# Kernel optimization log

Hardware: AMD Instinct MI355X
Metric: run time of the kernel (lower is better)

Reference implementation:

```python
import jax, jax.numpy as jnp
import numpy as np

B, T, D = 2, 1024, 1024
NUM_HEADS_ARG = 16
HS = D // NUM_HEADS_ARG          # 64 (per-head size)
H = HS                           # bug in source: num_heads passed = head_size -> 64 heads
FF = 4 * D
EPS = 1e-5


def _layernorm(x, gamma, beta):
    mu = jnp.mean(x, axis=-1, keepdims=True)
    var = jnp.mean(jnp.square(x - mu), axis=-1, keepdims=True)
    return (x - mu) * jax.lax.rsqrt(var + EPS) * gamma + beta


def setup_inputs() -> dict:
    key = jax.random.key(0)
    ks = jax.random.split(key, 12)
    s_d = 1.0 / np.sqrt(D)
    s_cat = 1.0 / np.sqrt(H * HS)
    s_ff = 1.0 / np.sqrt(FF)
    return {
        "x": jax.random.normal(ks[0], (B, T, D), jnp.float32),
        "Wq": jax.random.uniform(ks[1], (H, D, HS), jnp.float32, -s_d, s_d),
        "Wk": jax.random.uniform(ks[2], (H, D, HS), jnp.float32, -s_d, s_d),
        "Wv": jax.random.uniform(ks[3], (H, D, HS), jnp.float32, -s_d, s_d),
        "Wo": jax.random.uniform(ks[4], (H * HS, D), jnp.float32, -s_cat, s_cat),
        "bo": jax.random.uniform(ks[5], (D,), jnp.float32, -s_cat, s_cat),
        "W1": jax.random.uniform(ks[6], (D, FF), jnp.float32, -s_d, s_d),
        "b1": jax.random.uniform(ks[7], (FF,), jnp.float32, -s_d, s_d),
        "W2": jax.random.uniform(ks[8], (FF, D), jnp.float32, -s_ff, s_ff),
        "b2": jax.random.uniform(ks[9], (D,), jnp.float32, -s_ff, s_ff),
        "g1": jnp.ones((D,), jnp.float32),
        "be1": jnp.zeros((D,), jnp.float32),
        "g2": jnp.ones((D,), jnp.float32),
        "be2": jnp.zeros((D,), jnp.float32),
    }


def reference(x, Wq, Wk, Wv, Wo, bo, W1, b1, W2, b2, g1, be1, g2, be2):
    # per-head projections (no bias): [B,H,T,hs]
    q = jnp.einsum('btd,hde->bhte', x, Wq)
    k = jnp.einsum('btd,hde->bhte', x, Wk)
    v = jnp.einsum('btd,hde->bhte', x, Wv)
    scores = jnp.einsum('bhte,bhse->bhts', q, k) / np.sqrt(HS)  # [B,H,T,T]
    causal = jnp.tril(jnp.ones((T, T), bool))
    scores = jnp.where(causal, scores, -jnp.inf)
    probs = jax.nn.softmax(scores, axis=-1)
    att = jnp.einsum('bhts,bhse->bhte', probs, v)               # [B,H,T,hs]
    # torch stack(dim=3) -> [B,T,hs,H] then flatten: index = d*H + h
    cat = jnp.transpose(att, (0, 2, 3, 1)).reshape(B, T, HS * H)
    mha = cat @ Wo + bo
    x1 = _layernorm(x + mha, g1, be1)
    ff = jax.nn.relu(x1 @ W1 + b1) @ W2 + b2
    return _layernorm(x1 + ff, g2, be2)
```

## Files before the change

kernel.cpp:

```cpp
#include <hip/hip_runtime.h>

typedef unsigned short u16;
typedef __bf16 bf16x8 __attribute__((ext_vector_type(8)));
typedef float f32x4 __attribute__((ext_vector_type(4)));

#define B_ 2
#define T_ 1024
#define D_ 1024
#define H_ 64
#define HS_ 64
#define FF_ 4096
#define SZ_QKV 8388608L
#define S_SCALE 0.1803368801111f

__device__ __forceinline__ float bf2f(u16 u) {
  union { unsigned int v; float f; } x; x.v = ((unsigned int)u) << 16; return x.f;
}
__device__ __forceinline__ u16 f2bf(float f) {
  union { float f; unsigned int v; } x; x.f = f;
  unsigned int r = x.v + 0x7fffu + ((x.v >> 16) & 1u);
  return (u16)(r >> 16);
}
__device__ __forceinline__ u16 f2bf_rtz(float f) {
  union { float f; unsigned int v; } x; x.f = f;
  return (u16)(x.v >> 16);
}

typedef __attribute__((address_space(3))) unsigned int lds_u32;
typedef __attribute__((address_space(1))) const unsigned int glb_u32;
__device__ __forceinline__ void gload_lds16(const void* g, void* l) {
  __builtin_amdgcn_global_load_lds((glb_u32*)g, (lds_u32*)l, 16, 0, 0);
}

__global__ __launch_bounds__(256) void prep(
    const float* __restrict__ x, const float* __restrict__ Wq,
    const float* __restrict__ Wk, const float* __restrict__ Wv,
    const float* __restrict__ Wo, const float* __restrict__ W1,
    const float* __restrict__ W2,
    u16* __restrict__ xb, u16* __restrict__ Wqkvt, u16* __restrict__ Wot,
    u16* __restrict__ W1t, u16* __restrict__ W2t)
{
  __shared__ float tile[64][65];
  int id = blockIdx.x;
  if (id < 1024) {
    const long i = ((long)id * 256 + threadIdx.x) * 8;
    float4 a = *(const float4*)(x + i);
    float4 b = *(const float4*)(x + i + 4);
    union { uint4 v; u16 u[8]; } o;
    o.u[0]=f2bf(a.x); o.u[1]=f2bf(a.y); o.u[2]=f2bf(a.z); o.u[3]=f2bf(a.w);
    o.u[4]=f2bf(b.x); o.u[5]=f2bf(b.y); o.u[6]=f2bf(b.z); o.u[7]=f2bf(b.w);
    *(uint4*)(xb + i) = o.v;
    return;
  }
  id -= 1024;
  const float* in; u16* out; long ibase, obase; int in_rs, out_rs, r0, c0;
  if (id < 3072) {
    const int w = id >> 10, rem = id & 1023;
    const int z = rem >> 4, rt = rem & 15;
    in = (w == 0) ? Wq : (w == 1) ? Wk : Wv;
    ibase = (long)z * 65536; in_rs = 64; r0 = rt * 64; c0 = 0;
    out = Wqkvt + (long)w * 4194304;
    obase = (long)z * 65536; out_rs = 1024;
  } else if (id < 4096) {
    const int rem = id - 3072;
    const int z = rem >> 4, ct = rem & 15;
    in = Wo; ibase = (long)z * 1024; in_rs = 65536; r0 = 0; c0 = ct * 64;
    out = Wot; obase = (long)z * 64; out_rs = 4096;
  } else if (id < 5120) {
    const int rem = id - 4096;
    const int rt = rem >> 6, ct = rem & 63;
    in = W1; ibase = 0; in_rs = 4096; r0 = rt * 64; c0 = ct * 64;
    out = W1t; obase = 0; out_rs = 1024;
  } else {
    const int rem = id - 5120;
    const int rt = rem >> 4, ct = rem & 15;
    in = W2; ibase = 0; in_rs = 1024; r0 = rt * 64; c0 = ct * 64;
    out = W2t; obase = 0; out_rs = 4096;
  }
  const int t = threadIdx.x, lr = t >> 4, lc4 = (t & 15) * 4;
  #pragma unroll
  for (int j = 0; j < 4; ++j) {
    float4 f = *(const float4*)(in + ibase + (long)(r0 + lr + j * 16) * in_rs + c0 + lc4);
    tile[lr + j * 16][lc4]     = f.x;
    tile[lr + j * 16][lc4 + 1] = f.y;
    tile[lr + j * 16][lc4 + 2] = f.z;
    tile[lr + j * 16][lc4 + 3] = f.w;
  }
  __syncthreads();
  const int cr = t >> 3, ch = t & 7;
  #pragma unroll
  for (int j2 = 0; j2 < 2; ++j2) {
    const int crr = cr + j2 * 32;
    union { uint4 v; u16 u[8]; } o;
    #pragma unroll
    for (int i = 0; i < 8; ++i) o.u[i] = f2bf(tile[ch * 8 + i][crr]);
    *(uint4*)(out + obase + (long)(c0 + crr) * out_rs + r0 + ch * 8) = o.v;
  }
}

template<int TM, int EPI>
__global__ __launch_bounds__(256) void gemm_k(
    const u16* __restrict__ A, const u16* __restrict__ Bt, u16* __restrict__ C,
    const float* __restrict__ bias, int K, int lda, int ldb, int koff, int ldc)
{
  constexpr int NR = (TM == 128) ? 4 : 2;
  constexpr int AIT = TM / 64;
  __shared__ __attribute__((aligned(16))) u16 As[TM * 32];
  __shared__ __attribute__((aligned(16))) u16 Bs[128 * 32];
  const int bm = blockIdx.x, bn = blockIdx.y, bz = blockIdx.z;
  const long ko = (long)bz * koff;
  const int tid = threadIdx.x, wave = tid >> 6, lane = tid & 63;
  const int quad = lane >> 4, l16 = lane & 15;
  const int wm = (TM == 128) ? (wave & 1) * 64 : 0;
  const int wn = (TM == 128) ? (wave >> 1) * 64 : wave * 32;

  f32x4 acc[4][NR];
  #pragma unroll
  for (int i = 0; i < 4; ++i)
    #pragma unroll
    for (int j = 0; j < NR; ++j) acc[i][j] = (f32x4){0, 0, 0, 0};

  const int nK = K >> 5;
  for (int kc = 0; kc < nK; ++kc) {
    const int k0 = kc << 5;
    #pragma unroll
    for (int jA = 0; jA < AIT; ++jA) {
      const int i = jA * 4 + wave;
      const int chunk = i * 64 + lane;
      gload_lds16(A + (long)(bm * TM + (chunk >> 2)) * lda + ko + k0 + (chunk & 3) * 8,
                  (u16*)As + i * 512);
    }
    #pragma unroll
    for (int jB = 0; jB < 2; ++jB) {
      const int i = jB * 4 + wave;
      const int chunk = i * 64 + lane;
      gload_lds16(Bt + (long)(bn * 128 + (chunk >> 2)) * ldb + ko + k0 + (chunk & 3) * 8,
                  (u16*)Bs + i * 512);
    }
    __syncthreads();
    bf16x8 a[4], b[NR];
    #pragma unroll
    for (int i = 0; i < 4; ++i)
      a[i] = *(const bf16x8*)&As[(wm + i * 16 + l16) * 32 + quad * 8];
    #pragma unroll
    for (int j = 0; j < NR; ++j)
      b[j] = *(const bf16x8*)&Bs[(wn + j * 16 + l16) * 32 + quad * 8];
    #pragma unroll
    for (int i = 0; i < 4; ++i)
      #pragma unroll
      for (int j = 0; j < NR; ++j)
        acc[i][j] = __builtin_amdgcn_mfma_f32_16x16x32_bf16(a[i], b[j], acc[i][j], 0, 0, 0);
    __syncthreads();
  }

  #pragma unroll
  for (int j = 0; j < NR; ++j) {
    const int col = bn * 128 + wn + j * 16 + l16;
    const float bval = (EPI == 0 || EPI == 1) ? bias[col] : 0.f;
    #pragma unroll
    for (int i = 0; i < 4; ++i) {
      #pragma unroll
      for (int r = 0; r < 4; ++r) {
        const int row = bm * TM + wm + i * 16 + quad * 4 + r;
        float vv = acc[i][j][r] + bval;
        if (EPI == 1) vv = fmaxf(vv, 0.f);
        if (EPI == 2) {
          const int which = col >> 12, rem = col & 4095;
          const int h = rem >> 6, e = rem & 63;
          const int bb = row >> 10, t = row & 1023;
          C[(long)which * SZ_QKV + ((long)((bb << 6) + h)) * 65536L + t * 64 + e] = f2bf(vv);
        } else if (EPI == 3) {
          ((float*)C)[(long)bz * 2097152 + (long)row * ldc + col] = vv;
        } else {
          C[(long)row * ldc + col] = f2bf(vv);
        }
      }
    }
  }
}

__global__ __launch_bounds__(256) void attn_flash(
    const u16* __restrict__ Q, const u16* __restrict__ Kg,
    const u16* __restrict__ V, u16* __restrict__ Om)
{
  __shared__ __attribute__((aligned(16))) u16 Ks[2][64][72];
  __shared__ __attribute__((aligned(16))) u16 Vs[2][64][72];
  __shared__ __attribute__((aligned(16))) u16 QP[4][16][72];
  const int bh = blockIdx.x;
  const int qt = gridDim.y - 1 - blockIdx.y;
  const int b = bh >> 6, h = bh & 63;
  const long base = (long)bh * (T_ * HS_);
  const int tid = threadIdx.x;
  const int wave = tid >> 6, lane = tid & 63, quad = lane >> 4, l16 = lane & 15;
  const int sm = tid >> 2, sc = (tid & 3) * 16;
  const int vswz = (sc >> 4) << 3;

  {
    const int qr = lane >> 3, qe = (lane & 7) * 8;
    #pragma unroll
    for (int j = 0; j < 2; ++j) {
      union { uint4 v; u16 u[8]; } a, o;
      a.v = *(const uint4*)(Q + base + (long)(qt * 64 + wave * 16 + qr + j * 8) * HS_ + qe);
      #pragma unroll
      for (int i = 0; i < 8; ++i) o.u[i] = f2bf(bf2f(a.u[i]) * S_SCALE);
      *(uint4*)&QP[wave][qr + j * 8][qe] = o.v;
    }
  }
  bf16x8 aq0 = *(const bf16x8*)&QP[wave][l16][quad * 8];
  bf16x8 aq1 = *(const bf16x8*)&QP[wave][l16][32 + quad * 8];

  float psum[4] = { 0.f, 0.f, 0.f, 0.f };
  f32x4 oacc[4] = { {0,0,0,0}, {0,0,0,0}, {0,0,0,0}, {0,0,0,0} };

  uint4 kA, kB, vA, vB;
  kA = *(const uint4*)(Kg + base + (long)sm * HS_ + sc);
  kB = *(const uint4*)(Kg + base + (long)sm * HS_ + sc + 8);
  vA = *(const uint4*)(V  + base + (long)sm * HS_ + sc);
  vB = *(const uint4*)(V  + base + (long)sm * HS_ + sc + 8);
  {
    *(uint4*)&Ks[0][sm][sc] = kA; *(uint4*)&Ks[0][sm][sc + 8] = kB;
    union { uint4 v; u16 u[8]; } t0, t1; t0.v = vA; t1.v = vB;
    #pragma unroll
    for (int i = 0; i < 8; ++i) Vs[0][sc + i][sm ^ vswz] = t0.u[i];
    #pragma unroll
    for (int i = 0; i < 8; ++i) Vs[0][sc + 8 + i][sm ^ vswz] = t1.u[i];
  }
  __syncthreads();

  for (int kt = 0; kt <= qt; ++kt) {
    const int cur = kt & 1;
    const bool pf = (kt < qt);
    if (pf) {
      const long nb = base + (long)((kt + 1) * 64 + sm) * HS_ + sc;
      kA = *(const uint4*)(Kg + nb); kB = *(const uint4*)(Kg + nb + 8);
      vA = *(const uint4*)(V  + nb); vB = *(const uint4*)(V  + nb + 8);
    }

    f32x4 sacc[4] = { {0,0,0,0}, {0,0,0,0}, {0,0,0,0}, {0,0,0,0} };
    #pragma unroll
    for (int nt = 0; nt < 4; ++nt) {
      bf16x8 b0 = *(const bf16x8*)&Ks[cur][nt * 16 + l16][quad * 8];
      bf16x8 b1 = *(const bf16x8*)&Ks[cur][nt * 16 + l16][32 + quad * 8];
      sacc[nt] = __builtin_amdgcn_mfma_f32_16x16x32_bf16(aq0, b0, sacc[nt], 0, 0, 0);
      sacc[nt] = __builtin_amdgcn_mfma_f32_16x16x32_bf16(aq1, b1, sacc[nt], 0, 0, 0);
    }

    if (kt == qt) {
      #pragma unroll
      for (int nt = 0; nt < 4; ++nt) {
        const int col = nt * 16 + l16;
        #pragma unroll
        for (int r = 0; r < 4; ++r) {
          const int row = wave * 16 + quad * 4 + r;
          float p = exp2f(sacc[nt][r]);
          p = (col <= row) ? p : 0.f;
          sacc[nt][r] = p; psum[r] += p;
        }
      }
    } else {
      #pragma unroll
      for (int nt = 0; nt < 4; ++nt)
        #pragma unroll
        for (int r = 0; r < 4; ++r) {
          const float p = exp2f(sacc[nt][r]);
          sacc[nt][r] = p; psum[r] += p;
        }
    }

    #pragma unroll
    for (int nt = 0; nt < 4; ++nt)
      #pragma unroll
      for (int r = 0; r < 4; ++r)
        QP[wave][quad * 4 + r][nt * 16 + l16] = f2bf_rtz(sacc[nt][r]);
    bf16x8 p0 = *(const bf16x8*)&QP[wave][l16][quad * 8];
    bf16x8 p1 = *(const bf16x8*)&QP[wave][l16][32 + quad * 8];

    #pragma unroll
    for (int et = 0; et < 4; ++et) {
      const int c0 = ((quad ^ et) * 8);
      bf16x8 b0 = *(const bf16x8*)&Vs[cur][et * 16 + l16][c0];
      bf16x8 b1 = *(const bf16x8*)&Vs[cur][et * 16 + l16][32 + c0];
      oacc[et] = __builtin_amdgcn_mfma_f32_16x16x32_bf16(p0, b0, oacc[et], 0, 0, 0);
      oacc[et] = __builtin_amdgcn_mfma_f32_16x16x32_bf16(p1, b1, oacc[et], 0, 0, 0);
    }

    if (pf) {
      const int nxt = 1 - cur;
      *(uint4*)&Ks[nxt][sm][sc] = kA; *(uint4*)&Ks[nxt][sm][sc + 8] = kB;
      union { uint4 v; u16 u[8]; } t0, t1; t0.v = vA; t1.v = vB;
      #pragma unroll
      for (int i = 0; i < 8; ++i) Vs[nxt][sc + i][sm ^ vswz] = t0.u[i];
      #pragma unroll
      for (int i = 0; i < 8; ++i) Vs[nxt][sc + 8 + i][sm ^ vswz] = t1.u[i];
    }
    __syncthreads();
  }

  #pragma unroll
  for (int off = 1; off < 16; off <<= 1)
    #pragma unroll
    for (int r = 0; r < 4; ++r)
      psum[r] += __shfl_xor(psum[r], off, 64);
  u16 (*Os)[72] = Ks[0];
  #pragma unroll
  for (int r = 0; r < 4; ++r) {
    const float rinv = 1.f / fmaxf(psum[r], 1e-20f);
    const int row = wave * 16 + quad * 4 + r;
    #pragma unroll
    for (int et = 0; et < 4; ++et)
      Os[row][et * 16 + l16] = f2bf(oacc[et][r] * rinv);
  }
  const int orow = wave * 16 + (lane >> 3), oe = (lane & 7) * 8;
  #pragma unroll
  for (int it = 0; it < 2; ++it) {
    const int rr = orow + it * 8;
    uint4 o = *(const uint4*)&Os[rr][oe];
    *(uint4*)(Om + ((long)(b * T_ + qt * 64 + rr)) * 4096 + h * 64 + oe) = o;
  }
}

template<int XBF, int OBF>
__global__ __launch_bounds__(256) void ln_sum4(
    const float* __restrict__ P4, const float* __restrict__ bias,
    const void* __restrict__ Xv, const float* __restrict__ g,
    const float* __restrict__ be, void* __restrict__ outv)
{
  __shared__ float red[8];
  const int row = blockIdx.x, tid = threadIdx.x;
  const long base = (long)row * D_;
  float v4[4]; float s = 0.f;
  #pragma unroll
  for (int j = 0; j < 4; ++j) {
    const int i = tid + j * 256;
    float acc = bias[i];
    #pragma unroll
    for (int p = 0; p < 4; ++p) acc += P4[(long)p * 2097152 + base + i];
    const float xval = XBF ? bf2f(((const u16*)Xv)[base + i]) : ((const float*)Xv)[base + i];
    v4[j] = xval + acc;
    s += v4[j];
  }
  #pragma unroll
  for (int off = 32; off > 0; off >>= 1) s += __shfl_down(s, off, 64);
  if ((tid & 63) == 0) red[tid >> 6] = s;
  __syncthreads();
  const float mu = (red[0] + red[1] + red[2] + red[3]) * (1.f / D_);
  float vs = 0.f;
  #pragma unroll
  for (int j = 0; j < 4; ++j) { const float d = v4[j] - mu; vs += d * d; }
  #pragma unroll
  for (int off = 32; off > 0; off >>= 1) vs += __shfl_down(vs, off, 64);
  __syncthreads();
  if ((tid & 63) == 0) red[tid >> 6] = vs;
  __syncthreads();
  const float rs = rsqrtf((red[0] + red[1] + red[2] + red[3]) * (1.f / D_) + 1e-5f);
  #pragma unroll
  for (int j = 0; j < 4; ++j) {
    const int i = tid + j * 256;
    const float o = (v4[j] - mu) * rs * g[i] + be[i];
    if (OBF) ((u16*)outv)[base + i] = f2bf(o);
    else     ((float*)outv)[base + i] = o;
  }
}

extern "C" void kernel_launch(void* const* d_in, const int* in_sizes, int n_in,
                              void* d_out, int out_size, void* d_ws, size_t ws_size,
                              hipStream_t stream) {
  const float* x   = (const float*)d_in[0];
  const float* Wq  = (const float*)d_in[1];
  const float* Wk  = (const float*)d_in[2];
  const float* Wv  = (const float*)d_in[3];
  const float* Wo  = (const float*)d_in[4];
  const float* bo  = (const float*)d_in[5];
  const float* W1  = (const float*)d_in[6];
  const float* b1  = (const float*)d_in[7];
  const float* W2  = (const float*)d_in[8];
  const float* b2  = (const float*)d_in[9];
  const float* g1  = (const float*)d_in[10];
  const float* be1 = (const float*)d_in[11];
  const float* g2  = (const float*)d_in[12];
  const float* be2 = (const float*)d_in[13];
  float* out = (float*)d_out;

  u16* ws = (u16*)d_ws;
  u16* xb    = ws;
  u16* Wqkvt = xb + 2097152;
  u16* Wot   = Wqkvt + 12582912;
  u16* W1t   = Wot + 4194304;
  u16* W2t   = W1t + 4194304;
  u16* q     = W2t + 4194304;
  u16* k     = q + SZ_QKV;
  u16* v     = k + SZ_QKV;
  u16* Om    = v + SZ_QKV;
  float* P1 = (float*)q;
  float* P2 = (float*)q;
  u16* x1  = v;
  u16* h1  = Om;

  dim3 blk(256);

  prep<<<dim3(7168), blk, 0, stream>>>(x, Wq, Wk, Wv, Wo, W1, W2,
                                       xb, Wqkvt, Wot, W1t, W2t);

  gemm_k<128, 2><<<dim3(16, 96), blk, 0, stream>>>(
      xb, Wqkvt, q, nullptr, 1024, 1024, 1024, 0, 0);

  attn_flash<<<dim3(128, 16), blk, 0, stream>>>(q, k, v, Om);

  gemm_k<64, 3><<<dim3(32, 8, 4), blk, 0, stream>>>(
      Om, Wot, (u16*)P1, nullptr, 1024, 4096, 4096, 1024, 1024);

  ln_sum4<0, 1><<<dim3(2048), blk, 0, stream>>>(P1, bo, x, g1, be1, x1);

  gemm_k<128, 1><<<dim3(16, 32), blk, 0, stream>>>(
      x1, W1t, h1, b1, 1024, 1024, 1024, 0, 4096);

  gemm_k<64, 3><<<dim3(32, 8, 4), blk, 0, stream>>>(
      h1, W2t, (u16*)P2, nullptr, 1024, 4096, 4096, 1024, 1024);

  ln_sum4<1, 0><<<dim3(2048), blk, 0, stream>>>(P2, b2, x1, g2, be2, out);

  (void)in_sizes; (void)n_in; (void)out_size; (void)ws_size;
}
```

Measured before the change: 390.4 us.

## Replace GEMM with 256x128 tile, triple-buffered LDS pipeline and swizzled layout

Replaces the single-buffered GEMM kernel with one that uses a larger 256x128 block tile, a three-stage LDS ring buffer, and prefetching two K-steps ahead with explicit vmcnt waits and a single barrier per iteration. The LDS layout is XOR-swizzled to cut bank conflicts, and the leading dimensions become template constants. The aim is to overlap global loads with MFMA work and raise arithmetic intensity per block. The larger tile shrinks the grid (e.g. 256 blocks for the split-K GEMMs) and raises register and LDS use, which may reduce occupancy or wave-level parallelism.

```diff
diff --git a/kernel.cpp b/kernel.cpp
--- a/kernel.cpp
+++ b/kernel.cpp
@@ -98,70 +98,84 @@
   }
 }
 
-template<int TM, int EPI>
-__global__ __launch_bounds__(256) void gemm_k(
+template<int EPI, int LDA, int LDB>
+__global__ __launch_bounds__(256, 2) void gemm2(
     const u16* __restrict__ A, const u16* __restrict__ Bt, u16* __restrict__ C,
-    const float* __restrict__ bias, int K, int lda, int ldb, int koff, int ldc)
+    const float* __restrict__ bias, int K, int koff, int ldc)
 {
-  constexpr int NR = (TM == 128) ? 4 : 2;
-  constexpr int AIT = TM / 64;
-  __shared__ __attribute__((aligned(16))) u16 As[TM * 32];
-  __shared__ __attribute__((aligned(16))) u16 Bs[128 * 32];
+  __shared__ __attribute__((aligned(16))) u16 As[3][256 * 32];
+  __shared__ __attribute__((aligned(16))) u16 Bs[3][128 * 32];
   const int bm = blockIdx.x, bn = blockIdx.y, bz = blockIdx.z;
   const long ko = (long)bz * koff;
   const int tid = threadIdx.x, wave = tid >> 6, lane = tid & 63;
   const int quad = lane >> 4, l16 = lane & 15;
-  const int wm = (TM == 128) ? (wave & 1) * 64 : 0;
-  const int wn = (TM == 128) ? (wave >> 1) * 64 : wave * 32;
-
-  f32x4 acc[4][NR];
-  #pragma unroll
-  for (int i = 0; i < 4; ++i)
-    #pragma unroll
-    for (int j = 0; j < NR; ++j) acc[i][j] = (f32x4){0, 0, 0, 0};
+  const int wm = (wave & 1) * 128;
+  const int wn = (wave >> 1) * 64;
+  const int srcswz = ((lane & 3) ^ ((lane >> 3) & 3)) * 8;
+  const int arr = lane >> 2;
+  const int cs8 = (quad ^ ((l16 >> 1) & 3)) * 8;
+  const u16* Arow = A + (long)(bm * 256) * LDA + ko + srcswz;
+  const u16* Brow = Bt + (long)(bn * 128) * LDB + ko + srcswz;
+
+  f32x4 acc[8][4];
+  #pragma unroll
+  for (int i = 0; i < 8; ++i)
+    #pragma unroll
+    for (int j = 0; j < 4; ++j) acc[i][j] = (f32x4){0.f, 0.f, 0.f, 0.f};
 
   const int nK = K >> 5;
-  for (int kc = 0; kc < nK; ++kc) {
-    const int k0 = kc << 5;
-    #pragma unroll
-    for (int jA = 0; jA < AIT; ++jA) {
-      const int i = jA * 4 + wave;
-      const int chunk = i * 64 + lane;
-      gload_lds16(A + (long)(bm * TM + (chunk >> 2)) * lda + ko + k0 + (chunk & 3) * 8,
-                  (u16*)As + i * 512);
-    }
-    #pragma unroll
-    for (int jB = 0; jB < 2; ++jB) {
-      const int i = jB * 4 + wave;
-      const int chunk = i * 64 + lane;
-      gload_lds16(Bt + (long)(bn * 128 + (chunk >> 2)) * ldb + ko + k0 + (chunk & 3) * 8,
-                  (u16*)Bs + i * 512);
-    }
-    __syncthreads();
-    bf16x8 a[4], b[NR];
-    #pragma unroll
-    for (int i = 0; i < 4; ++i)
-      a[i] = *(const bf16x8*)&As[(wm + i * 16 + l16) * 32 + quad * 8];
-    #pragma unroll
-    for (int j = 0; j < NR; ++j)
-      b[j] = *(const bf16x8*)&Bs[(wn + j * 16 + l16) * 32 + quad * 8];
-    #pragma unroll
-    for (int i = 0; i < 4; ++i)
-      #pragma unroll
-      for (int j = 0; j < NR; ++j)
+
+  auto STAGE = [&](int buf, int t) {
+    const int k0 = t << 5;
+    #pragma unroll
+    for (int it = 0; it < 4; ++it) {
+      const int i = it * 4 + wave;
+      gload_lds16(Arow + (long)(i * 16 + arr) * LDA + k0, (u16*)As[buf] + i * 512);
+    }
+    #pragma unroll
+    for (int it = 0; it < 2; ++it) {
+      const int i = it * 4 + wave;
+      gload_lds16(Brow + (long)(i * 16 + arr) * LDB + k0, (u16*)Bs[buf] + i * 512);
+    }
+  };
+
+  STAGE(0, 0);
+  STAGE(1, 1);
+  int cc = 0, cs = 2;
+  for (int t = 0; t < nK; ++t) {
+    if (t < nK - 1) asm volatile("s_waitcnt vmcnt(6)" ::: "memory");
+    else            asm volatile("s_waitcnt vmcnt(0)" ::: "memory");
+    __builtin_amdgcn_sched_barrier(0);
+    __builtin_amdgcn_s_barrier();
+    __builtin_amdgcn_sched_barrier(0);
+    if (t + 2 < nK) STAGE(cs, t + 2);
+    const u16* At = As[cc];
+    const u16* Bl = Bs[cc];
+    bf16x8 a[8], b[4];
+    #pragma unroll
+    for (int j = 0; j < 4; ++j)
+      b[j] = *(const bf16x8*)&Bl[(wn + j * 16 + l16) * 32 + cs8];
+    #pragma unroll
+    for (int i = 0; i < 8; ++i)
+      a[i] = *(const bf16x8*)&At[(wm + i * 16 + l16) * 32 + cs8];
+    #pragma unroll
+    for (int i = 0; i < 8; ++i)
+      #pragma unroll
+      for (int j = 0; j < 4; ++j)
         acc[i][j] = __builtin_amdgcn_mfma_f32_16x16x32_bf16(a[i], b[j], acc[i][j], 0, 0, 0);
-    __syncthreads();
-  }
-
-  #pragma unroll
-  for (int j = 0; j < NR; ++j) {
+    cc = (cc == 2) ? 0 : cc + 1;
+    cs = (cs == 2) ? 0 : cs + 1;
+  }
+
+  #pragma unroll
+  for (int j = 0; j < 4; ++j) {
     const int col = bn * 128 + wn + j * 16 + l16;
-    const float bval = (EPI == 0 || EPI == 1) ? bias[col] : 0.f;
-    #pragma unroll
-    for (int i = 0; i < 4; ++i) {
+    const float bval = (EPI == 1) ? bias[col] : 0.f;
+    #pragma unroll
+    for (int i = 0; i < 8; ++i) {
       #pragma unroll
       for (int r = 0; r < 4; ++r) {
-        const int row = bm * TM + wm + i * 16 + quad * 4 + r;
+        const int row = bm * 256 + wm + i * 16 + quad * 4 + r;
         float vv = acc[i][j][r] + bval;
         if (EPI == 1) vv = fmaxf(vv, 0.f);
         if (EPI == 2) {
@@ -401,21 +415,21 @@
   prep<<<dim3(7168), blk, 0, stream>>>(x, Wq, Wk, Wv, Wo, W1, W2,
                                        xb, Wqkvt, Wot, W1t, W2t);
 
-  gemm_k<128, 2><<<dim3(16, 96), blk, 0, stream>>>(
-      xb, Wqkvt, q, nullptr, 1024, 1024, 1024, 0, 0);
+  gemm2<2, 1024, 1024><<<dim3(8, 96), blk, 0, stream>>>(
+      xb, Wqkvt, q, nullptr, 1024, 0, 0);
 
   attn_flash<<<dim3(128, 16), blk, 0, stream>>>(q, k, v, Om);
 
-  gemm_k<64, 3><<<dim3(32, 8, 4), blk, 0, stream>>>(
-      Om, Wot, (u16*)P1, nullptr, 1024, 4096, 4096, 1024, 1024);
+  gemm2<3, 4096, 4096><<<dim3(8, 8, 4), blk, 0, stream>>>(
+      Om, Wot, (u16*)P1, nullptr, 1024, 1024, 1024);
 
   ln_sum4<0, 1><<<dim3(2048), blk, 0, stream>>>(P1, bo, x, g1, be1, x1);
 
-  gemm_k<128, 1><<<dim3(16, 32), blk, 0, stream>>>(
-      x1, W1t, h1, b1, 1024, 1024, 1024, 0, 4096);
-
-  gemm_k<64, 3><<<dim3(32, 8, 4), blk, 0, stream>>>(
-      h1, W2t, (u16*)P2, nullptr, 1024, 4096, 4096, 1024, 1024);
+  gemm2<1, 1024, 1024><<<dim3(8, 32), blk, 0, stream>>>(
+      x1, W1t, h1, b1, 1024, 0, 4096);
+
+  gemm2<3, 4096, 4096><<<dim3(8, 8, 4), blk, 0, stream>>>(
+      h1, W2t, (u16*)P2, nullptr, 1024, 1024, 1024);
 
   ln_sum4<1, 0><<<dim3(2048), blk, 0, stream>>>(P2, b2, x1, g2, be2, out);
 
```

Result: slower. 405.6 us (+3.9%).
